# Kernel tuning notes

Hardware: AMD Instinct MI355X
Metric: run time of the kernel (lower is better)

Reference implementation:

```python
import jax, jax.numpy as jnp
import numpy as np

B, S, D, H = 2, 2048, 1024, 16
Dh = D // H
ROPE_BASE = 10000.0


def _rope_cos_sin(seq_len, dh, dtype):
    inv_freq = 1.0 / (ROPE_BASE ** (jnp.arange(0, dh, 2, dtype=jnp.float32) / dh))
    t = jnp.arange(seq_len, dtype=jnp.float32)
    freqs = jnp.outer(t, inv_freq)              # (S, Dh/2)
    emb = jnp.concatenate([freqs, freqs], -1)   # (S, Dh)
    return jnp.cos(emb).astype(dtype), jnp.sin(emb).astype(dtype)


def _rotate_half(x):
    x1, x2 = jnp.split(x, 2, axis=-1)
    return jnp.concatenate([-x2, x1], axis=-1)


def setup_inputs() -> dict:
    key = jax.random.key(0)
    k1, k2, k3 = jax.random.split(key, 3)
    x = jax.random.normal(k1, (B, S, D), dtype=jnp.float32)
    w_qkv = jax.random.normal(k2, (D, 3 * D), dtype=jnp.float32) * (1.0 / np.sqrt(D))
    w_proj = jax.random.normal(k3, (D, D), dtype=jnp.float32) * (1.0 / np.sqrt(D))
    return {"x": x, "w_qkv": w_qkv, "w_proj": w_proj}


def reference(x, w_qkv, w_proj):
    b, s, d = x.shape
    qkv = x @ w_qkv                              # (B, S, 3D)
    q, k, v = jnp.split(qkv, 3, axis=-1)
    # (B, S, D) -> (B, H, S, Dh)
    shape_heads = lambda t: t.reshape(b, s, H, Dh).transpose(0, 2, 1, 3)
    q, k, v = shape_heads(q), shape_heads(k), shape_heads(v)
    cos, sin = _rope_cos_sin(s, Dh, x.dtype)     # (S, Dh) each
    cos = cos[None, None]                        # (1,1,S,Dh)
    sin = sin[None, None]
    q = q * cos + _rotate_half(q) * sin
    k = k * cos + _rotate_half(k) * sin
    attn = jnp.einsum('bhqd,bhkd->bhqk', q, k) / np.sqrt(Dh).astype(x.dtype)
    causal_mask = jnp.tril(jnp.ones((s, s), dtype=bool))
    attn = jnp.where(causal_mask, attn, -jnp.inf)
    attn = jax.nn.softmax(attn, axis=-1)
    out = jnp.einsum('bhqk,bhkd->bhqd', attn, v)
    out = out.transpose(0, 2, 1, 3).reshape(b, s, d)
    return out @ w_proj
```

## Files before the change

### kernel.cpp

```cpp
#include <hip/hip_runtime.h>


typedef unsigned short u16;
typedef unsigned int u32;
typedef __bf16 bf16x8 __attribute__((ext_vector_type(8)));
typedef unsigned short u16x8 __attribute__((ext_vector_type(8)));
typedef unsigned short u16x4 __attribute__((ext_vector_type(4)));
typedef float f32x4 __attribute__((ext_vector_type(4)));

#define B_ 2
#define S_ 2048
#define D_ 1024
#define H_ 16
#define DH_ 64
#define BS_ (B_ * S_)
#define N3_ (3 * D_)

__device__ __forceinline__ u16 f2bf(float f) {
  unsigned u = __float_as_uint(f);
  u += 0x7FFFu + ((u >> 16) & 1u);
  return (u16)(u >> 16);
}
__device__ __forceinline__ float bf2f(u16 s) {
  return __uint_as_float(((unsigned)s) << 16);
}

union BU { u16x8 u; bf16x8 b; u32 w[4]; };

__device__ __forceinline__ void gl16(const void* g, void* l) {
  __builtin_amdgcn_global_load_lds(
      (const __attribute__((address_space(1))) u32*)g,
      (__attribute__((address_space(3))) u32*)l, 16, 0, 0);
}

__global__ __launch_bounds__(256) void k_pre(const float* __restrict__ x,
                                             const float* __restrict__ wqkv,
                                             const float* __restrict__ wproj,
                                             u16* __restrict__ xb,
                                             u16* __restrict__ wqkvT,
                                             u16* __restrict__ wprojT,
                                             float* __restrict__ ct,
                                             float* __restrict__ st) {
  __shared__ float tl[32][33];
  const int bid = blockIdx.x;
  const int t = threadIdx.x;
  if (bid < 4096) {
    const int i = bid * 256 + t;
    const float4 f = ((const float4*)x)[i];
    u16x4 o;
    o[0] = f2bf(f.x); o[1] = f2bf(f.y); o[2] = f2bf(f.z); o[3] = f2bf(f.w);
    *(u16x4*)(xb + (size_t)i * 4) = o;
    return;
  }
  if (bid < 8192) {
    const float* w; u16* wT; int R, C, bx, by;
    if (bid < 7168) {
      w = wqkv; wT = wqkvT; R = D_; C = N3_;
      const int id2 = bid - 4096; bx = id2 % 96; by = id2 / 96;
    } else {
      w = wproj; wT = wprojT; R = D_; C = D_;
      const int id2 = bid - 7168; bx = id2 % 32; by = id2 / 32;
    }
    const int lrow = t >> 3, seg = t & 7;
    const int r0 = by * 32, c0 = bx * 32;
    const float4 f = *(const float4*)(w + (size_t)(r0 + lrow) * C + c0 + seg * 4);
    tl[lrow][seg * 4 + 0] = f.x; tl[lrow][seg * 4 + 1] = f.y;
    tl[lrow][seg * 4 + 2] = f.z; tl[lrow][seg * 4 + 3] = f.w;
    __syncthreads();
    u16x4 o;
#pragma unroll
    for (int j = 0; j < 4; ++j) o[j] = f2bf(tl[seg * 4 + j][lrow]);
    *(u16x4*)(wT + (size_t)(c0 + lrow) * R + r0 + seg * 4) = o;
    return;
  }
  {
    const int idx = (bid - 8192) * 256 + t;
    const int tpos = idx >> 5, i = idx & 31;
    const float invf = powf(10000.0f, -(float)i * (1.0f / 32.0f));
    const float a = (float)tpos * invf;
    ct[idx] = cosf(a);
    st[idx] = sinf(a);
  }
}

template <typename OutT>
__global__ __launch_bounds__(256) void k_gemm(const u16* __restrict__ A,
                                              const u16* __restrict__ BT,
                                              OutT* __restrict__ C,
                                              int M, int N, int K, int nbx) {
  __shared__ u16 smem[16384];
  u16* laA = smem;
  u16* laB = smem + 8192;
  const int t = threadIdx.x;
  const int per_x = gridDim.x >> 3;
  const int nid = (blockIdx.x & 7) * per_x + (blockIdx.x >> 3);
  const int n0 = (nid % nbx) * 128, m0 = (nid / nbx) * 128;
  const int w = t >> 6, lane = t & 63;
  const int lr = lane & 15, lg = lane >> 4;
  const int wm = (w >> 1) * 64, wn = (w & 1) * 64;
  const int NK = K >> 5;

  const int srow = lane >> 2;
  const int sc = ((lane & 3) ^ ((lane >> 3) & 3)) * 8;
  const u16* Ag = A + (size_t)(m0 + w * 32 + srow) * K + sc;
  const u16* Bg = BT + (size_t)(n0 + w * 32 + srow) * K + sc;
  const int ldsw = w * 1024;

  f32x4 acc[4][4] = {};

#pragma unroll
  for (int i = 0; i < 2; ++i) {
    gl16(Ag + (size_t)i * 16 * K, laA + ldsw + i * 512);
    gl16(Bg + (size_t)i * 16 * K, laB + ldsw + i * 512);
  }
  __syncthreads();

  int cur = 0;
  for (int kt = 0; kt < NK; ++kt) {
    if (kt + 1 < NK) {
      const int ko = (kt + 1) * 32;
#pragma unroll
      for (int i = 0; i < 2; ++i) {
        gl16(Ag + (size_t)i * 16 * K + ko, laA + (cur ^ 1) * 4096 + ldsw + i * 512);
        gl16(Bg + (size_t)i * 16 * K + ko, laB + (cur ^ 1) * 4096 + ldsw + i * 512);
      }
    }
    const char* pa = (const char*)(laA + cur * 4096);
    const char* pb = (const char*)(laB + cur * 4096);
    BU af[4], bfr[4];
    const int rsw = ((lr >> 1) & 3);
#pragma unroll
    for (int mi = 0; mi < 4; ++mi) {
      const int ra = wm + mi * 16 + lr;
      af[mi].u = *(const u16x8*)(pa + ra * 64 + ((lg ^ rsw) * 16));
      const int rb = wn + mi * 16 + lr;
      bfr[mi].u = *(const u16x8*)(pb + rb * 64 + ((lg ^ rsw) * 16));
    }
#pragma unroll
    for (int mi = 0; mi < 4; ++mi)
#pragma unroll
      for (int ni = 0; ni < 4; ++ni)
        acc[mi][ni] = __builtin_amdgcn_mfma_f32_16x16x32_bf16(af[mi].b, bfr[ni].b,
                                                              acc[mi][ni], 0, 0, 0);
    __syncthreads();
    cur ^= 1;
  }

  if constexpr (sizeof(OutT) == 2) {
    u16* ew = smem + w * 4096;
#pragma unroll
    for (int mi = 0; mi < 4; ++mi)
#pragma unroll
      for (int ni = 0; ni < 4; ++ni)
#pragma unroll
        for (int r = 0; r < 4; ++r)
          ew[(mi * 16 + lg * 4 + r) * 64 + ni * 16 + lr] = f2bf(acc[mi][ni][r]);
    const int er = lane >> 3, es = (lane & 7) * 8;
#pragma unroll
    for (int pass = 0; pass < 8; ++pass) {
      const int row = pass * 8 + er;
      const u16x8 v = *(const u16x8*)(ew + row * 64 + es);
      *(u16x8*)((u16*)C + (size_t)(m0 + wm + row) * N + n0 + wn + es) = v;
    }
  } else {
#pragma unroll
    for (int mi = 0; mi < 4; ++mi)
#pragma unroll
      for (int ni = 0; ni < 4; ++ni)
#pragma unroll
        for (int r = 0; r < 4; ++r) {
          const int row = m0 + wm + mi * 16 + lg * 4 + r;
          const int col = n0 + wn + ni * 16 + lr;
          ((float*)C)[(size_t)row * N + col] = acc[mi][ni][r];
        }
  }
}

__global__ __launch_bounds__(256) void k_prep(const u16* __restrict__ qkv,
                                              const float* __restrict__ ct,
                                              const float* __restrict__ st,
                                              u16* __restrict__ Q, u16* __restrict__ K,
                                              u16* __restrict__ Vt) {
  __shared__ u16 vl[64][72];
  const int bid = blockIdx.x;
  const int xcd = bid & 7, slot = bid >> 3;
  const int bh = xcd + 8 * (slot >> 5);
  const int stile = slot & 31;
  const int b = bh >> 4, h = bh & 15;
  const int t = threadIdx.x;
  const int row = t >> 2, qr = t & 3;
  const int s = stile * 64 + row;
  const u16* base = qkv + (size_t)(b * S_ + s) * N3_ + h * DH_;
  const int d0 = qr * 8;
  float c[8], sn[8];
#pragma unroll
  for (int j = 0; j < 8; ++j) {
    c[j] = ct[s * 32 + d0 + j];
    sn[j] = st[s * 32 + d0 + j];
  }
#pragma unroll
  for (int part = 0; part < 2; ++part) {
    const float qs = (part == 0) ? 0.125f : 1.0f;
    const u16* src = base + part * D_;
    u16x8 lo = *(const u16x8*)(src + d0);
    u16x8 hi = *(const u16x8*)(src + d0 + 32);
    u16x8 olo, ohi;
#pragma unroll
    for (int j = 0; j < 8; ++j) {
      float x1 = bf2f(lo[j]) * qs, x2 = bf2f(hi[j]) * qs;
      olo[j] = f2bf(x1 * c[j] - x2 * sn[j]);
      ohi[j] = f2bf(x2 * c[j] + x1 * sn[j]);
    }
    u16* dst = (part ? K : Q) + ((size_t)bh * S_ + s) * DH_;
    *(u16x8*)(dst + d0) = olo;
    *(u16x8*)(dst + d0 + 32) = ohi;
  }
  u16x8 v0 = *(const u16x8*)(base + 2 * D_ + qr * 16);
  u16x8 v1 = *(const u16x8*)(base + 2 * D_ + qr * 16 + 8);
#pragma unroll
  for (int j = 0; j < 8; ++j) {
    vl[qr * 16 + j][row] = v0[j];
    vl[qr * 16 + 8 + j][row] = v1[j];
  }
  __syncthreads();
  const int dh = row, sc = qr * 16;
  u16x8 o0, o1;
#pragma unroll
  for (int j = 0; j < 8; ++j) { o0[j] = vl[dh][sc + j]; o1[j] = vl[dh][sc + 8 + j]; }
  u16* vdst = Vt + ((size_t)bh * DH_ + dh) * S_ + stile * 64 + sc;
  *(u16x8*)vdst = o0;
  *(u16x8*)(vdst + 8) = o1;
}

__global__ __launch_bounds__(256, 2) void k_attn(const u16* __restrict__ Q,
                                                 const u16* __restrict__ K,
                                                 const u16* __restrict__ Vt,
                                                 u16* __restrict__ Ao) {
  __shared__ char kvb_[2][16384];
  const int bid = blockIdx.x;
  const int xcd = bid & 7, inner = bid >> 3;
  const int bh = xcd + 8 * (inner & 3);
  const int qt = 31 - (inner >> 2);
  const int t = threadIdx.x;
  const int w = t >> 6, lane = t & 63;
  const int lr = lane & 15, lg = lane >> 4;
  const int q0 = qt * 64 + w * 16;
  const int nt = qt + 1;

  const u16* Kbh = K + (size_t)bh * S_ * DH_;
  const u16* Vbh = Vt + (size_t)bh * DH_ * S_;

  const int sr = lane >> 3;
  const int sc = ((lane & 7) ^ sr) * 8;
  char* kd0 = kvb_[0] + w * 2048;
  char* kd1 = kvb_[1] + w * 2048;
  int prow[2], vrow[2];
#pragma unroll
  for (int j = 0; j < 2; ++j) {
    const int a = w * 16 + j * 8 + sr;
    prow[j] = (((a >> 4) & 1) << 5) | (((a >> 2) & 3) << 3) |
              (((a >> 5) & 1) << 2) | (a & 3);
    vrow[j] = a;
  }

  const u16* Qb = Q + ((size_t)bh * S_ + q0) * DH_;
  BU qf0, qf1;
  qf0.u = *(const u16x8*)(Qb + lr * DH_ + lg * 8);
  qf1.u = *(const u16x8*)(Qb + lr * DH_ + 32 + lg * 8);

  f32x4 o[4] = {};
  float m = -1e30f, l = 0.f;

#pragma unroll
  for (int j = 0; j < 2; ++j) {
    gl16(Kbh + (size_t)prow[j] * DH_ + sc, kd0 + j * 1024);
    gl16(Vbh + (size_t)vrow[j] * S_ + sc, kd0 + 8192 + j * 1024);
  }
  __syncthreads();

  int cur = 0;
  for (int it = 0; it < nt; ++it) {
    const int kv0 = it * 64;
    if (it + 1 < nt) {
      const int kvn = kv0 + 64;
      char* nd = cur ? kd0 : kd1;
#pragma unroll
      for (int j = 0; j < 2; ++j) {
        gl16(Kbh + (size_t)(kvn + prow[j]) * DH_ + sc, nd + j * 1024);
        gl16(Vbh + (size_t)vrow[j] * S_ + kvn + sc, nd + 8192 + j * 1024);
      }
    }
    const char* base = kvb_[cur];
    f32x4 s[4] = {};
#pragma unroll
    for (int kvbi = 0; kvbi < 4; ++kvbi) {
      const int row = kvbi * 16 + lr;
      const int sw = (lr & 7) << 4;
      BU k0, k1;
      k0.u = *(const u16x8*)(base + row * 128 + ((lg * 16) ^ sw));
      k1.u = *(const u16x8*)(base + row * 128 + ((64 + lg * 16) ^ sw));
      s[kvbi] = __builtin_amdgcn_mfma_f32_16x16x32_bf16(k0.b, qf0.b, s[kvbi], 0, 0, 0);
      s[kvbi] = __builtin_amdgcn_mfma_f32_16x16x32_bf16(k1.b, qf1.b, s[kvbi], 0, 0, 0);
    }
    float p[16];
#pragma unroll
    for (int kvbi = 0; kvbi < 4; ++kvbi)
#pragma unroll
      for (int r = 0; r < 4; ++r) p[kvbi * 4 + r] = s[kvbi][r];
    if (it == nt - 1) {
#pragma unroll
      for (int kvbi = 0; kvbi < 4; ++kvbi)
#pragma unroll
        for (int r = 0; r < 4; ++r) {
          const int tkv = ((kvbi & 1) << 5) + lg * 8 + ((kvbi >> 1) << 2) + r;
          if (kv0 + tkv > q0 + lr) p[kvbi * 4 + r] = -1e30f;
        }
    }
    float a0 = fmaxf(p[0], p[1]),   a1 = fmaxf(p[2], p[3]);
    float a2 = fmaxf(p[4], p[5]),   a3 = fmaxf(p[6], p[7]);
    float a4 = fmaxf(p[8], p[9]),   a5 = fmaxf(p[10], p[11]);
    float a6 = fmaxf(p[12], p[13]), a7 = fmaxf(p[14], p[15]);
    a0 = fmaxf(a0, a1); a2 = fmaxf(a2, a3); a4 = fmaxf(a4, a5); a6 = fmaxf(a6, a7);
    const float mx = fmaxf(fmaxf(a0, a2), fmaxf(a4, a6));
    if (__any(mx > m + 8.f)) {
      float cm = mx;
      cm = fmaxf(cm, __shfl_xor(cm, 16, 64));
      cm = fmaxf(cm, __shfl_xor(cm, 32, 64));
      const float mn = fmaxf(m, cm);
      const float al = __expf(m - mn);
      m = mn;
      l *= al;
#pragma unroll
      for (int d = 0; d < 4; ++d)
#pragma unroll
        for (int r = 0; r < 4; ++r) o[d][r] *= al;
    }
#pragma unroll
    for (int i = 0; i < 16; ++i) p[i] = __expf(p[i] - m);
    {
      float s0 = (p[0] + p[1]) + (p[2] + p[3]);
      float s1 = (p[4] + p[5]) + (p[6] + p[7]);
      float s2 = (p[8] + p[9]) + (p[10] + p[11]);
      float s3 = (p[12] + p[13]) + (p[14] + p[15]);
      l += (s0 + s1) + (s2 + s3);
    }
    BU pf0, pf1;
    pf0.u[0] = f2bf(p[0]);  pf0.u[1] = f2bf(p[1]);
    pf0.u[2] = f2bf(p[2]);  pf0.u[3] = f2bf(p[3]);
    pf0.u[4] = f2bf(p[8]);  pf0.u[5] = f2bf(p[9]);
    pf0.u[6] = f2bf(p[10]); pf0.u[7] = f2bf(p[11]);
    pf1.u[0] = f2bf(p[4]);  pf1.u[1] = f2bf(p[5]);
    pf1.u[2] = f2bf(p[6]);  pf1.u[3] = f2bf(p[7]);
    pf1.u[4] = f2bf(p[12]); pf1.u[5] = f2bf(p[13]);
    pf1.u[6] = f2bf(p[14]); pf1.u[7] = f2bf(p[15]);
#pragma unroll
    for (int d = 0; d < 4; ++d) {
      const int row = d * 16 + lr;
      const int sw = (lr & 7) << 4;
      BU v0, v1;
      v0.u = *(const u16x8*)(base + 8192 + row * 128 + ((lg * 16) ^ sw));
      v1.u = *(const u16x8*)(base + 8192 + row * 128 + ((64 + lg * 16) ^ sw));
      o[d] = __builtin_amdgcn_mfma_f32_16x16x32_bf16(v0.b, pf0.b, o[d], 0, 0, 0);
      o[d] = __builtin_amdgcn_mfma_f32_16x16x32_bf16(v1.b, pf1.b, o[d], 0, 0, 0);
    }
    __syncthreads();
    cur ^= 1;
  }

  l += __shfl_xor(l, 16, 64);
  l += __shfl_xor(l, 32, 64);
  const float inv = 1.0f / l;
  const int b = bh >> 4, h = bh & 15;
  const size_t rowo = ((size_t)b * S_ + q0 + lr) * D_ + h * DH_;
#pragma unroll
  for (int d = 0; d < 4; ++d) {
    u16x4 w4;
#pragma unroll
    for (int r = 0; r < 4; ++r) w4[r] = f2bf(o[d][r] * inv);
    *(u16x4*)(Ao + rowo + d * 16 + lg * 4) = w4;
  }
}

extern "C" void kernel_launch(void* const* d_in, const int* in_sizes, int n_in,
                              void* d_out, int out_size, void* d_ws, size_t ws_size,
                              hipStream_t stream) {
  const float* x = (const float*)d_in[0];
  const float* wqkv = (const float*)d_in[1];
  const float* wproj = (const float*)d_in[2];
  float* out = (float*)d_out;
  char* ws = (char*)d_ws;

  u16* xb      = (u16*)(ws + 0);
  u16* wqkvT   = (u16*)(ws + 8388608);
  u16* wprojT  = (u16*)(ws + 14680064);
  u16* qkvb    = (u16*)(ws + 16777216);
  u16* Qb      = (u16*)(ws + 41943040);
  u16* Kb      = (u16*)(ws + 50331648);
  u16* Vtb     = (u16*)(ws + 58720256);
  u16* aob     = (u16*)(ws + 67108864);
  float* ct    = (float*)(ws + 75497472);
  float* stab  = (float*)(ws + 75759616);

  k_pre<<<8448, 256, 0, stream>>>(x, wqkv, wproj, xb, wqkvT, wprojT, ct, stab);
  k_gemm<u16><<<768, 256, 0, stream>>>(xb, wqkvT, qkvb, BS_, N3_, D_, 24);
  k_prep<<<1024, 256, 0, stream>>>(qkvb, ct, stab, Qb, Kb, Vtb);
  k_attn<<<1024, 256, 0, stream>>>(Qb, Kb, Vtb, aob);
  k_gemm<float><<<256, 256, 0, stream>>>(aob, wprojT, out, BS_, D_, D_, 8);
}
```

Baseline: 110.7 us.

## Fuse RoPE, Q/K/V head split and V transpose into QKV GEMM epilogue

The QKV GEMM epilogue now stages each warp's 64x64 tile in swizzled LDS and writes Q and K with RoPE and the Q scale applied, plus V already transposed, straight into the per-head layouts. This removes the intermediate bf16 qkv buffer round trip through global memory and the separate k_prep launch. In exchange the GEMM epilogue does more work and reads the cos/sin tables, and the rounding order changes slightly because the Q scale is now applied after RoPE.

Result: slower. 114.8 us (+3.8%).

```diff
diff --git a/kernel.cpp b/kernel.cpp
--- a/kernel.cpp
+++ b/kernel.cpp
@@ -83,11 +83,10 @@
   }
 }
 
-template <typename OutT>
-__global__ __launch_bounds__(256) void k_gemm(const u16* __restrict__ A,
-                                              const u16* __restrict__ BT,
-                                              OutT* __restrict__ C,
-                                              int M, int N, int K, int nbx) {
+__global__ __launch_bounds__(256) void k_gemm_f32(const u16* __restrict__ A,
+                                                  const u16* __restrict__ BT,
+                                                  float* __restrict__ C,
+                                                  int M, int N, int K, int nbx) {
   __shared__ u16 smem[16384];
   u16* laA = smem;
   u16* laB = smem + 8192;
@@ -146,90 +145,150 @@
     cur ^= 1;
   }
 
-  if constexpr (sizeof(OutT) == 2) {
-    u16* ew = smem + w * 4096;
+#pragma unroll
+  for (int mi = 0; mi < 4; ++mi)
+#pragma unroll
+    for (int ni = 0; ni < 4; ++ni)
+#pragma unroll
+      for (int r = 0; r < 4; ++r) {
+        const int row = m0 + wm + mi * 16 + lg * 4 + r;
+        const int col = n0 + wn + ni * 16 + lr;
+        C[(size_t)row * N + col] = acc[mi][ni][r];
+      }
+}
+
+__global__ __launch_bounds__(256) void k_gemm_qkv(const u16* __restrict__ A,
+                                                  const u16* __restrict__ BT,
+                                                  const float* __restrict__ ct,
+                                                  const float* __restrict__ st,
+                                                  u16* __restrict__ Qb,
+                                                  u16* __restrict__ Kb,
+                                                  u16* __restrict__ Vt) {
+  __shared__ u16 smem[16384];
+  u16* laA = smem;
+  u16* laB = smem + 8192;
+  const int t = threadIdx.x;
+  const int per_x = gridDim.x >> 3;
+  const int nid = (blockIdx.x & 7) * per_x + (blockIdx.x >> 3);
+  const int n0 = (nid % 24) * 128, m0 = (nid / 24) * 128;
+  const int w = t >> 6, lane = t & 63;
+  const int lr = lane & 15, lg = lane >> 4;
+  const int wm = (w >> 1) * 64, wn = (w & 1) * 64;
+  const int NK = D_ >> 5;
+
+  const int srow = lane >> 2;
+  const int sc = ((lane & 3) ^ ((lane >> 3) & 3)) * 8;
+  const u16* Ag = A + (size_t)(m0 + w * 32 + srow) * D_ + sc;
+  const u16* Bg = BT + (size_t)(n0 + w * 32 + srow) * D_ + sc;
+  const int ldsw = w * 1024;
+
+  f32x4 acc[4][4] = {};
+
+#pragma unroll
+  for (int i = 0; i < 2; ++i) {
+    gl16(Ag + (size_t)i * 16 * D_, laA + ldsw + i * 512);
+    gl16(Bg + (size_t)i * 16 * D_, laB + ldsw + i * 512);
+  }
+  __syncthreads();
+
+  int cur = 0;
+  for (int kt = 0; kt < NK; ++kt) {
+    if (kt + 1 < NK) {
+      const int ko = (kt + 1) * 32;
+#pragma unroll
+      for (int i = 0; i < 2; ++i) {
+        gl16(Ag + (size_t)i * 16 * D_ + ko, laA + (cur ^ 1) * 4096 + ldsw + i * 512);
+        gl16(Bg + (size_t)i * 16 * D_ + ko, laB + (cur ^ 1) * 4096 + ldsw + i * 512);
+      }
+    }
+    const char* pa = (const char*)(laA + cur * 4096);
+    const char* pb = (const char*)(laB + cur * 4096);
+    BU af[4], bfr[4];
+    const int rsw = ((lr >> 1) & 3);
+#pragma unroll
+    for (int mi = 0; mi < 4; ++mi) {
+      const int ra = wm + mi * 16 + lr;
+      af[mi].u = *(const u16x8*)(pa + ra * 64 + ((lg ^ rsw) * 16));
+      const int rb = wn + mi * 16 + lr;
+      bfr[mi].u = *(const u16x8*)(pb + rb * 64 + ((lg ^ rsw) * 16));
+    }
 #pragma unroll
     for (int mi = 0; mi < 4; ++mi)
 #pragma unroll
       for (int ni = 0; ni < 4; ++ni)
-#pragma unroll
-        for (int r = 0; r < 4; ++r)
-          ew[(mi * 16 + lg * 4 + r) * 64 + ni * 16 + lr] = f2bf(acc[mi][ni][r]);
-    const int er = lane >> 3, es = (lane & 7) * 8;
+        acc[mi][ni] = __builtin_amdgcn_mfma_f32_16x16x32_bf16(af[mi].b, bfr[ni].b,
+                                                              acc[mi][ni], 0, 0, 0);
+    __syncthreads();
+    cur ^= 1;
+  }
+
+  const int c0 = n0 + wn;
+  const int part = c0 >> 10;
+  const int h = (c0 & 1023) >> 6;
+  const int s_base = m0 + wm;
+  const int b = s_base >> 11;
+  const int sl0 = s_base & 2047;
+  const int bh = b * 16 + h;
+  u16* ew = smem + w * 4096;
+
+  if (part < 2) {
+#pragma unroll
+    for (int mi = 0; mi < 4; ++mi)
+#pragma unroll
+      for (int ni = 0; ni < 4; ++ni)
+#pragma unroll
+        for (int r = 0; r < 4; ++r) {
+          const int sl = mi * 16 + lg * 4 + r;
+          const int dh = ni * 16 + lr;
+          ew[sl * 64 + (dh ^ ((sl & 7) << 3))] = f2bf(acc[mi][ni][r]);
+        }
+    u16* dst = (part == 0 ? Qb : Kb) + (size_t)bh * S_ * DH_;
+    const float qs = (part == 0) ? 0.125f : 1.0f;
+    const int er = lane >> 2, ko = lane & 3;
+#pragma unroll
+    for (int pass = 0; pass < 4; ++pass) {
+      const int row = pass * 16 + er;
+      const int swz = (row & 7) << 3;
+      const int sg = sl0 + row;
+      const u16x8 vlo = *(const u16x8*)(ew + row * 64 + ((ko * 8) ^ swz));
+      const u16x8 vhi = *(const u16x8*)(ew + row * 64 + ((32 + ko * 8) ^ swz));
+      const float4 cA = *(const float4*)(ct + sg * 32 + ko * 8);
+      const float4 cB = *(const float4*)(ct + sg * 32 + ko * 8 + 4);
+      const float4 sA = *(const float4*)(st + sg * 32 + ko * 8);
+      const float4 sB = *(const float4*)(st + sg * 32 + ko * 8 + 4);
+      const float cc[8] = {cA.x, cA.y, cA.z, cA.w, cB.x, cB.y, cB.z, cB.w};
+      const float ss[8] = {sA.x, sA.y, sA.z, sA.w, sB.x, sB.y, sB.z, sB.w};
+      u16x8 olo, ohi;
+#pragma unroll
+      for (int j = 0; j < 8; ++j) {
+        const float x1 = bf2f(vlo[j]), x2 = bf2f(vhi[j]);
+        olo[j] = f2bf((x1 * cc[j] - x2 * ss[j]) * qs);
+        ohi[j] = f2bf((x2 * cc[j] + x1 * ss[j]) * qs);
+      }
+      *(u16x8*)(dst + (size_t)sg * DH_ + ko * 8) = olo;
+      *(u16x8*)(dst + (size_t)sg * DH_ + 32 + ko * 8) = ohi;
+    }
+  } else {
+#pragma unroll
+    for (int mi = 0; mi < 4; ++mi)
+#pragma unroll
+      for (int ni = 0; ni < 4; ++ni)
+#pragma unroll
+        for (int r = 0; r < 4; r += 2) {
+          const int sl = mi * 16 + lg * 4 + r;
+          const int dh = ni * 16 + lr;
+          const u32 two = (u32)f2bf(acc[mi][ni][r]) |
+                          ((u32)f2bf(acc[mi][ni][r + 1]) << 16);
+          *(u32*)((char*)ew + (size_t)(dh * 64 + (sl ^ ((dh & 7) << 3))) * 2) = two;
+        }
+    const int er2 = lane >> 3, ks = (lane & 7) * 8;
 #pragma unroll
     for (int pass = 0; pass < 8; ++pass) {
-      const int row = pass * 8 + er;
-      const u16x8 v = *(const u16x8*)(ew + row * 64 + es);
-      *(u16x8*)((u16*)C + (size_t)(m0 + wm + row) * N + n0 + wn + es) = v;
-    }
-  } else {
-#pragma unroll
-    for (int mi = 0; mi < 4; ++mi)
-#pragma unroll
-      for (int ni = 0; ni < 4; ++ni)
-#pragma unroll
-        for (int r = 0; r < 4; ++r) {
-          const int row = m0 + wm + mi * 16 + lg * 4 + r;
-          const int col = n0 + wn + ni * 16 + lr;
-          ((float*)C)[(size_t)row * N + col] = acc[mi][ni][r];
-        }
-  }
-}
-
-__global__ __launch_bounds__(256) void k_prep(const u16* __restrict__ qkv,
-                                              const float* __restrict__ ct,
-                                              const float* __restrict__ st,
-                                              u16* __restrict__ Q, u16* __restrict__ K,
-                                              u16* __restrict__ Vt) {
-  __shared__ u16 vl[64][72];
-  const int bid = blockIdx.x;
-  const int xcd = bid & 7, slot = bid >> 3;
-  const int bh = xcd + 8 * (slot >> 5);
-  const int stile = slot & 31;
-  const int b = bh >> 4, h = bh & 15;
-  const int t = threadIdx.x;
-  const int row = t >> 2, qr = t & 3;
-  const int s = stile * 64 + row;
-  const u16* base = qkv + (size_t)(b * S_ + s) * N3_ + h * DH_;
-  const int d0 = qr * 8;
-  float c[8], sn[8];
-#pragma unroll
-  for (int j = 0; j < 8; ++j) {
-    c[j] = ct[s * 32 + d0 + j];
-    sn[j] = st[s * 32 + d0 + j];
-  }
-#pragma unroll
-  for (int part = 0; part < 2; ++part) {
-    const float qs = (part == 0) ? 0.125f : 1.0f;
-    const u16* src = base + part * D_;
-    u16x8 lo = *(const u16x8*)(src + d0);
-    u16x8 hi = *(const u16x8*)(src + d0 + 32);
-    u16x8 olo, ohi;
-#pragma unroll
-    for (int j = 0; j < 8; ++j) {
-      float x1 = bf2f(lo[j]) * qs, x2 = bf2f(hi[j]) * qs;
-      olo[j] = f2bf(x1 * c[j] - x2 * sn[j]);
-      ohi[j] = f2bf(x2 * c[j] + x1 * sn[j]);
-    }
-    u16* dst = (part ? K : Q) + ((size_t)bh * S_ + s) * DH_;
-    *(u16x8*)(dst + d0) = olo;
-    *(u16x8*)(dst + d0 + 32) = ohi;
-  }
-  u16x8 v0 = *(const u16x8*)(base + 2 * D_ + qr * 16);
-  u16x8 v1 = *(const u16x8*)(base + 2 * D_ + qr * 16 + 8);
-#pragma unroll
-  for (int j = 0; j < 8; ++j) {
-    vl[qr * 16 + j][row] = v0[j];
-    vl[qr * 16 + 8 + j][row] = v1[j];
-  }
-  __syncthreads();
-  const int dh = row, sc = qr * 16;
-  u16x8 o0, o1;
-#pragma unroll
-  for (int j = 0; j < 8; ++j) { o0[j] = vl[dh][sc + j]; o1[j] = vl[dh][sc + 8 + j]; }
-  u16* vdst = Vt + ((size_t)bh * DH_ + dh) * S_ + stile * 64 + sc;
-  *(u16x8*)vdst = o0;
-  *(u16x8*)(vdst + 8) = o1;
+      const int dh = pass * 8 + er2;
+      const u16x8 v = *(const u16x8*)(ew + dh * 64 + (ks ^ ((dh & 7) << 3)));
+      *(u16x8*)(Vt + ((size_t)bh * DH_ + dh) * S_ + sl0 + ks) = v;
+    }
+  }
 }
 
 __global__ __launch_bounds__(256, 2) void k_attn(const u16* __restrict__ Q,
@@ -393,17 +452,15 @@
   u16* xb      = (u16*)(ws + 0);
   u16* wqkvT   = (u16*)(ws + 8388608);
   u16* wprojT  = (u16*)(ws + 14680064);
-  u16* qkvb    = (u16*)(ws + 16777216);
-  u16* Qb      = (u16*)(ws + 41943040);
-  u16* Kb      = (u16*)(ws + 50331648);
-  u16* Vtb     = (u16*)(ws + 58720256);
-  u16* aob     = (u16*)(ws + 67108864);
-  float* ct    = (float*)(ws + 75497472);
-  float* stab  = (float*)(ws + 75759616);
+  u16* Qb      = (u16*)(ws + 16777216);
+  u16* Kb      = (u16*)(ws + 25165824);
+  u16* Vtb     = (u16*)(ws + 33554432);
+  u16* aob     = (u16*)(ws + 41943040);
+  float* ct    = (float*)(ws + 50331648);
+  float* stab  = (float*)(ws + 50593792);
 
   k_pre<<<8448, 256, 0, stream>>>(x, wqkv, wproj, xb, wqkvT, wprojT, ct, stab);
-  k_gemm<u16><<<768, 256, 0, stream>>>(xb, wqkvT, qkvb, BS_, N3_, D_, 24);
-  k_prep<<<1024, 256, 0, stream>>>(qkvb, ct, stab, Qb, Kb, Vtb);
+  k_gemm_qkv<<<768, 256, 0, stream>>>(xb, wqkvT, ct, stab, Qb, Kb, Vtb);
   k_attn<<<1024, 256, 0, stream>>>(Qb, Kb, Vtb, aob);
-  k_gemm<float><<<256, 256, 0, stream>>>(aob, wprojT, out, BS_, D_, D_, 8);
-}
+  k_gemm_f32<<<256, 256, 0, stream>>>(aob, wprojT, out, BS_, D_, D_, 8);
+}
```
